# Kernel optimization log

Hardware: AMD Instinct MI355X
Metric: run time of the kernel (lower is better)

## Reference

```python
import jax, jax.numpy as jnp
import numpy as np

IN_F = 256
OUT_F = 128
ALPHA = 0.2  # LeakyReLU negative slope
NEG_INF = -9.0e15


def setup_inputs() -> dict:
    key = jax.random.key(0)
    k_h, k_j, k_adj, k_w1, k_w2, k_a = jax.random.split(key, 6)
    B, N = 8, 2048
    h = jax.random.normal(k_h, (B, N, IN_F), dtype=jnp.float32)
    j = jax.random.normal(k_j, (B, N, IN_F), dtype=jnp.float32)
    adj = jax.random.randint(k_adj, (B, N, N), 0, 2, dtype=jnp.int32)
    # xavier_uniform with gain=1.414: bound = gain * sqrt(6/(fan_in+fan_out))
    def xavier(k, shape, gain=1.414):
        bound = gain * np.sqrt(6.0 / (shape[0] + shape[1]))
        return jax.random.uniform(k, shape, jnp.float32, -bound, bound)
    W1 = xavier(k_w1, (IN_F, OUT_F))
    W2 = xavier(k_w2, (IN_F, OUT_F))
    a = xavier(k_a, (2 * OUT_F, 1))
    return {"h": h, "j": j, "adj": adj, "W1": W1, "W2": W2, "a": a}


def reference(h, j, adj, W1, W2, a):
    # Projections: [B, N, OUT_F]
    Wh = jnp.einsum("bnf,fo->bno", h, W1)
    Wj = jnp.einsum("bnf,fo->bno", j, W2)
    # Additive attention logits: e[b,i,k] = leakyrelu(Wh@a1 [i] + Wh@a2 [k])
    Wh1 = Wh @ a[:OUT_F, :]   # [B, N, 1]
    Wh2 = Wh @ a[OUT_F:, :]   # [B, N, 1]
    e = jax.nn.leaky_relu(Wh1 + jnp.swapaxes(Wh2, 1, 2), negative_slope=ALPHA)
    # Mask non-edges, row-softmax over neighbors (dim=2)
    logits = jnp.where(adj > 0, e, NEG_INF)
    attention = jax.nn.softmax(logits, axis=2)
    # dropout skipped (eval mode). attention@Wh + attention@Wj == attention@(Wh+Wj)
    output = jnp.einsum("bik,bko->bio", attention, Wh + Wj)
    return jax.nn.elu(output)  # concat=True
```

## Files before the change

### kernel.cpp

```cpp
#include <hip/hip_runtime.h>
#include <hip/hip_bf16.h>

#define BATCH 8
#define NN 2048
#define IN_F 256
#define OUT_F 128
#define ALPHA 0.2f

typedef __attribute__((ext_vector_type(8))) short short8v;
typedef __attribute__((ext_vector_type(4))) float f32x4;

static __device__ __forceinline__ unsigned short f2bf(float x) {
    unsigned int u = __float_as_uint(x);
    u = (u + 0x7fffu + ((u >> 16) & 1u)) >> 16;
    return (unsigned short)u;
}

static __device__ __forceinline__ unsigned long long pk4(float a, float b, float c, float d) {
    union { unsigned long long ll; __hip_bfloat162 h2[2]; } u;
    u.h2[0] = __float22bfloat162_rn(make_float2(a, b));
    u.h2[1] = __float22bfloat162_rn(make_float2(c, d));
    return u.ll;
}

__global__ __launch_bounds__(256) void k_prew(
    const float* __restrict__ W1, const float* __restrict__ W2,
    const float* __restrict__ a,
    unsigned short* __restrict__ Wt, float* __restrict__ w1a1, float* __restrict__ w1a2)
{
    const int t = threadIdx.x;
    const int k8 = blockIdx.x * 8;
#pragma unroll
    for (int q = 0; q < 4; ++q) {
        const int idx = q * 256 + t;
        const int o = idx & 127;
        const int kk = k8 + (idx >> 7);
        const float v = (kk < IN_F) ? W1[kk * OUT_F + o] : W2[(kk - IN_F) * OUT_F + o];
        Wt[(size_t)o * 512 + kk] = f2bf(v);
    }
    if (k8 < IN_F) {
        const int lane = t & 63, w = t >> 6;
#pragma unroll
        for (int u = 0; u < 2; ++u) {
            const int kk = k8 + 2 * w + u;
            const float* wr = W1 + kk * OUT_F;
            float v1 = wr[lane] * a[lane] + wr[lane + 64] * a[lane + 64];
            float v2 = wr[lane] * a[OUT_F + lane] + wr[lane + 64] * a[OUT_F + lane + 64];
#pragma unroll
            for (int off = 32; off; off >>= 1) {
                v1 += __shfl_xor(v1, off);
                v2 += __shfl_xor(v2, off);
            }
            if (lane == 0) { w1a1[kk] = v1; w1a2[kk] = v2; }
        }
    }
}

#define BM 16

__global__ __launch_bounds__(256) void k_proj(
    const float* __restrict__ h, const float* __restrict__ j,
    const unsigned short* __restrict__ Wt,
    const float* __restrict__ w1a1g, const float* __restrict__ w1a2g,
    const int* __restrict__ adj,
    unsigned short* __restrict__ Vf, float* __restrict__ s1, float* __restrict__ s2,
    unsigned short* __restrict__ bits16)
{
    __shared__ __align__(16) unsigned short X[BM * 512];

    const int t = threadIdx.x, lane = t & 63, w = t >> 6;
    const int row0 = blockIdx.x * BM;
    const int b = row0 >> 11, n0 = row0 & 2047;

    const float4* wa1v = (const float4*)w1a1g;
    const float4* wa2v = (const float4*)w1a2g;

    const int srow = w * 4 + (lane >> 4);
    const int scol = lane & 15;
    const int sswz = (srow & 7) << 4;
    const float* hrow = h + (size_t)(row0 + srow) * IN_F;
    const float* jrow = j + (size_t)(row0 + srow) * IN_F;

    float d1 = 0.f, d2 = 0.f;
#pragma unroll
    for (int q = 0; q < 4; ++q) {
        const int f4 = q * 16 + scol;
        const float4 hv = ((const float4*)hrow)[f4];
        *(unsigned long long*)((char*)X + ((srow * 1024 + f4 * 8) ^ sswz)) =
            pk4(hv.x, hv.y, hv.z, hv.w);
        const float4 a1 = wa1v[f4], a2 = wa2v[f4];
        d1 += hv.x * a1.x + hv.y * a1.y + hv.z * a1.z + hv.w * a1.w;
        d2 += hv.x * a2.x + hv.y * a2.y + hv.z * a2.z + hv.w * a2.w;
    }
#pragma unroll
    for (int q = 0; q < 4; ++q) {
        const int f4 = q * 16 + scol;
        const float4 jv = ((const float4*)jrow)[f4];
        *(unsigned long long*)((char*)X + ((srow * 1024 + 512 + f4 * 8) ^ sswz)) =
            pk4(jv.x, jv.y, jv.z, jv.w);
    }
    d1 += __shfl_xor(d1, 1); d1 += __shfl_xor(d1, 2);
    d1 += __shfl_xor(d1, 4); d1 += __shfl_xor(d1, 8);
    d2 += __shfl_xor(d2, 1); d2 += __shfl_xor(d2, 2);
    d2 += __shfl_xor(d2, 4); d2 += __shfl_xor(d2, 8);
    if (scol == 0) { s1[row0 + srow] = d1; s2[row0 + srow] = d2; }
    __syncthreads();

    const unsigned short* wb = Wt + (size_t)(w * 32 + (lane & 15)) * 512 + ((lane >> 4) * 8);
    const int abase = (lane & 15) * 1024 + ((lane >> 4) * 16);
    const int aswz = (lane & 7) << 4;

    f32x4 acc0 = {0.f, 0.f, 0.f, 0.f}, acc1 = {0.f, 0.f, 0.f, 0.f};
#pragma unroll
    for (int ks = 0; ks < 16; ++ks) {
        const short8v af = *(const short8v*)((const char*)X + ((abase + ks * 64) ^ aswz));
        const short8v b0 = *(const short8v*)(wb + ks * 32);
        const short8v b1 = *(const short8v*)(wb + 16 * 512 + ks * 32);
        acc0 = __builtin_amdgcn_mfma_f32_16x16x32_bf16(af, b0, acc0, 0, 0, 0);
        acc1 = __builtin_amdgcn_mfma_f32_16x16x32_bf16(af, b1, acc1, 0, 0, 0);
    }

    const int nn = n0 + (lane >> 4) * 4;
    const size_t vbase = (size_t)b * 524288
                       + ((size_t)(nn >> 5) << 13)
                       + (((nn & 31) >> 3) << 4) + ((nn & 7) << 1);
#pragma unroll
    for (int f = 0; f < 2; ++f) {
        const f32x4 ac = f ? acc1 : acc0;
        const int o = w * 32 + f * 16 + (lane & 15);
        *(unsigned long long*)((char*)Vf + vbase + o * 64) = pk4(ac[0], ac[1], ac[2], ac[3]);
    }

    const int gstride = 1024 * 256;
    for (int g = blockIdx.x * 256 + t; g < (BATCH * NN * NN) / 16; g += gstride) {
        const int4* ap = (const int4*)(adj + (size_t)g * 16);
        const int4 x0 = ap[0], x1 = ap[1], x2 = ap[2], x3 = ap[3];
        unsigned m = 0;
        m |= (x0.x > 0) ? 1u : 0u;        m |= (x0.y > 0) ? 2u : 0u;
        m |= (x0.z > 0) ? 4u : 0u;        m |= (x0.w > 0) ? 8u : 0u;
        m |= (x1.x > 0) ? 16u : 0u;       m |= (x1.y > 0) ? 32u : 0u;
        m |= (x1.z > 0) ? 64u : 0u;       m |= (x1.w > 0) ? 128u : 0u;
        m |= (x2.x > 0) ? 256u : 0u;      m |= (x2.y > 0) ? 512u : 0u;
        m |= (x2.z > 0) ? 1024u : 0u;     m |= (x2.w > 0) ? 2048u : 0u;
        m |= (x3.x > 0) ? 4096u : 0u;     m |= (x3.y > 0) ? 8192u : 0u;
        m |= (x3.z > 0) ? 16384u : 0u;    m |= (x3.w > 0) ? 32768u : 0u;
        bits16[g] = (unsigned short)m;
    }
}

#define IBLK 32

__global__ __launch_bounds__(256, 3) void k_attn(
    const unsigned char* __restrict__ bits, const unsigned short* __restrict__ Vf,
    const float* __restrict__ s1g, const float* __restrict__ s2g,
    float* __restrict__ out)
{
    __shared__ __align__(16) char smem[33792];
    __shared__ float rs_lds[4][IBLK];
    __shared__ float wmaxs[4];
    __shared__ __align__(16) float lut[16][4];

    float* s2_lds = (float*)smem;
    unsigned int* bitw = (unsigned int*)(smem + 8192);
    float* comb = (float*)smem;

    const int t = threadIdx.x, lane = t & 63, w = t >> 6;
    const int orig = blockIdx.x;
    const int b = orig & 7;
    const int r = orig >> 3;
    const int oh = r >> 6;
    const int i0 = (r & 63) * IBLK;

    if (t < 16) {
        lut[t][0] = (float)(t & 1);
        lut[t][1] = (float)((t >> 1) & 1);
        lut[t][2] = (float)((t >> 2) & 1);
        lut[t][3] = (float)((t >> 3) & 1);
    }

    {
        const unsigned int* bg = (const unsigned int*)(bits + ((size_t)b * NN + i0) * 256);
#pragma unroll
        for (int q = 0; q < 8; ++q) {
            const int idx = q * 256 + t;
            bitw[(idx >> 6) * 65 + (idx & 63)] = bg[idx];
        }
    }

    const float4* s2v = (const float4*)(s2g + b * NN);
    float lmax = -1e30f;
#pragma unroll
    for (int q = 0; q < 2; ++q) {
        const int idx = q * 256 + t;
        const float4 v = s2v[idx];
        ((float4*)s2_lds)[idx] = v;
        lmax = fmaxf(fmaxf(lmax, fmaxf(v.x, v.y)), fmaxf(v.z, v.w));
    }
#pragma unroll
    for (int off = 32; off; off >>= 1) lmax = fmaxf(lmax, __shfl_xor(lmax, off));
    if (lane == 0) wmaxs[w] = lmax;

    const int irow = lane & 15;
    const int kcb = lane >> 4;
    const int kw = w * 512;

    const float s1r0 = s1g[b * NN + i0 + irow];
    const float s1r1 = s1g[b * NN + i0 + 16 + irow];
    __syncthreads();
    const float s2max = fmaxf(fmaxf(wmaxs[0], wmaxs[1]), fmaxf(wmaxs[2], wmaxs[3]));
    const float mx0 = s1r0 + s2max, mx1 = s1r1 + s2max;
    const float mA0 = fmaxf(mx0, ALPHA * mx0);
    const float mA1 = fmaxf(mx1, ALPHA * mx1);

    const float* s2p = s2_lds + kw + kcb * 8;
    const char* vfb = (const char*)Vf + (size_t)b * 524288 + (size_t)(w * 16) * 8192
                    + (size_t)(oh * 64 + irow) * 64 + (size_t)kcb * 16;
    const unsigned int* bw0p = bitw + irow * 65 + w * 16;
    const unsigned int* bw1p = bitw + (16 + irow) * 65 + w * 16;

    short8v vone;
#pragma unroll
    for (int q = 0; q < 8; ++q) vone[q] = (short)0x3F80;

    f32x4 acc0[4], acc1[4];
    f32x4 acc_ps0 = {0.f, 0.f, 0.f, 0.f}, acc_ps1 = {0.f, 0.f, 0.f, 0.f};
#pragma unroll
    for (int og = 0; og < 4; ++og) {
        acc0[og] = (f32x4){0.f, 0.f, 0.f, 0.f};
        acc1[og] = (f32x4){0.f, 0.f, 0.f, 0.f};
    }

#pragma unroll
    for (int ks = 0; ks < 16; ++ks) {
        const char* vk = vfb + (size_t)ks * 8192;
        const short8v vf0 = *(const short8v*)(vk);
        const short8v vf1 = *(const short8v*)(vk + 1024);
        const short8v vf2 = *(const short8v*)(vk + 2048);
        const short8v vf3 = *(const short8v*)(vk + 3072);

        const unsigned int bb0 = (bw0p[ks] >> (kcb * 8)) & 0xffu;
        const unsigned int bb1 = (bw1p[ks] >> (kcb * 8)) & 0xffu;
        const float4 m00 = ((const float4*)lut)[bb0 & 15], m01 = ((const float4*)lut)[bb0 >> 4];
        const float4 m10 = ((const float4*)lut)[bb1 & 15], m11 = ((const float4*)lut)[bb1 >> 4];

        const float4 sa = *(const float4*)(s2p + ks * 32);
        const float4 sb = *(const float4*)(s2p + ks * 32 + 4);
        const float s2r[8] = {sa.x, sa.y, sa.z, sa.w, sb.x, sb.y, sb.z, sb.w};
        const float mk0[8] = {m00.x, m00.y, m00.z, m00.w, m01.x, m01.y, m01.z, m01.w};
        const float mk1[8] = {m10.x, m10.y, m10.z, m10.w, m11.x, m11.y, m11.z, m11.w};

        float p0[8], p1[8];
#pragma unroll
        for (int e = 0; e < 8; ++e) {
            float x0 = s1r0 + s2r[e];
            x0 = fmaxf(x0, ALPHA * x0);
            p0[e] = __expf(x0 - mA0) * mk0[e];
            float x1 = s1r1 + s2r[e];
            x1 = fmaxf(x1, ALPHA * x1);
            p1[e] = __expf(x1 - mA1) * mk1[e];
        }
        union { short8v v; __hip_bfloat162 h2[4]; } pb0, pb1;
#pragma unroll
        for (int q = 0; q < 4; ++q) {
            pb0.h2[q] = __float22bfloat162_rn(make_float2(p0[2 * q], p0[2 * q + 1]));
            pb1.h2[q] = __float22bfloat162_rn(make_float2(p1[2 * q], p1[2 * q + 1]));
        }

        acc_ps0 = __builtin_amdgcn_mfma_f32_16x16x32_bf16(vone, pb0.v, acc_ps0, 0, 0, 0);
        acc_ps1 = __builtin_amdgcn_mfma_f32_16x16x32_bf16(vone, pb1.v, acc_ps1, 0, 0, 0);
        acc0[0] = __builtin_amdgcn_mfma_f32_16x16x32_bf16(vf0, pb0.v, acc0[0], 0, 0, 0);
        acc1[0] = __builtin_amdgcn_mfma_f32_16x16x32_bf16(vf0, pb1.v, acc1[0], 0, 0, 0);
        acc0[1] = __builtin_amdgcn_mfma_f32_16x16x32_bf16(vf1, pb0.v, acc0[1], 0, 0, 0);
        acc1[1] = __builtin_amdgcn_mfma_f32_16x16x32_bf16(vf1, pb1.v, acc1[1], 0, 0, 0);
        acc0[2] = __builtin_amdgcn_mfma_f32_16x16x32_bf16(vf2, pb0.v, acc0[2], 0, 0, 0);
        acc1[2] = __builtin_amdgcn_mfma_f32_16x16x32_bf16(vf2, pb1.v, acc1[2], 0, 0, 0);
        acc0[3] = __builtin_amdgcn_mfma_f32_16x16x32_bf16(vf3, pb0.v, acc0[3], 0, 0, 0);
        acc1[3] = __builtin_amdgcn_mfma_f32_16x16x32_bf16(vf3, pb1.v, acc1[3], 0, 0, 0);
    }

    if (lane < 16) {
        rs_lds[w][lane] = acc_ps0[0];
        rs_lds[w][16 + lane] = acc_ps1[0];
    }

    __syncthreads();
#pragma unroll
    for (int og = 0; og < 4; ++og) {
#pragma unroll
        for (int rr = 0; rr < 4; ++rr) {
            const int ol = og * 16 + kcb * 4 + rr;
            comb[(w * 64 + ol) * 33 + irow] = acc0[og][rr];
            comb[(w * 64 + ol) * 33 + 16 + irow] = acc1[og][rr];
        }
    }
    __syncthreads();

    const int i = t >> 3, oc = t & 7;
    const float tot = rs_lds[0][i] + rs_lds[1][i] + rs_lds[2][i] + rs_lds[3][i];
    const float inv = 1.0f / tot;
    float res[8];
#pragma unroll
    for (int u = 0; u < 8; ++u) {
        const int ol = oc * 8 + u;
        float v = comb[ol * 33 + i] + comb[(64 + ol) * 33 + i]
                + comb[(128 + ol) * 33 + i] + comb[(192 + ol) * 33 + i];
        v *= inv;
        res[u] = (v > 0.f) ? v : expm1f(v);
    }
    float4* ob = (float4*)(out + ((size_t)b * NN + i0 + i) * OUT_F + oh * 64 + oc * 8);
    ob[0] = make_float4(res[0], res[1], res[2], res[3]);
    ob[1] = make_float4(res[4], res[5], res[6], res[7]);
}

extern "C" void kernel_launch(void* const* d_in, const int* in_sizes, int n_in,
                              void* d_out, int out_size, void* d_ws, size_t ws_size,
                              hipStream_t stream) {
    const float* h  = (const float*)d_in[0];
    const float* j  = (const float*)d_in[1];
    const int* adj  = (const int*)d_in[2];
    const float* W1 = (const float*)d_in[3];
    const float* W2 = (const float*)d_in[4];
    const float* a  = (const float*)d_in[5];
    float* out = (float*)d_out;

    char* ws = (char*)d_ws;
    unsigned short* Vf = (unsigned short*)ws;
    ws += (size_t)BATCH * OUT_F * NN * 2;
    float* s1 = (float*)ws; ws += (size_t)BATCH * NN * 4;
    float* s2 = (float*)ws; ws += (size_t)BATCH * NN * 4;
    unsigned short* Wt = (unsigned short*)ws; ws += 128 * 512 * 2;
    float* w1a1 = (float*)ws; ws += 512 * 4;
    float* w1a2 = (float*)ws; ws += 512 * 4;
    unsigned char* bits = (unsigned char*)ws;

    k_prew<<<64, 256, 0, stream>>>(W1, W2, a, Wt, w1a1, w1a2);
    k_proj<<<(BATCH * NN) / BM, 256, 0, stream>>>(h, j, Wt, w1a1, w1a2, adj,
                                                  Vf, s1, s2, (unsigned short*)bits);
    k_attn<<<(BATCH * NN) / IBLK * 2, 256, 0, stream>>>(bits, Vf, s1, s2, out);
}
```

Baseline: 68.74 us.

## Double attention row tile to 64 rows per block, reusing V fragments

Each attention block now covers 64 query rows instead of 32, so every V fragment loaded from global memory feeds four row groups of MFMAs instead of two. The aim is to halve V traffic per output and amortise the shared s2 and bitmask setup over more rows. The cost is twice the accumulator registers, occupancy hint lowered from 3 to 2 blocks, and an epilogue that reduces through LDS in two serialized passes with extra barriers. This relies on the launch grid shrinking to match the new row indexing.

After: 70.80 us. +3.0%, slower.

```diff
diff --git a/kernel.cpp b/kernel.cpp
--- a/kernel.cpp
+++ b/kernel.cpp
@@ -148,9 +148,9 @@
     }
 }
 
-#define IBLK 32
-
-__global__ __launch_bounds__(256, 3) void k_attn(
+#define IBLK 64
+
+__global__ __launch_bounds__(256, 2) void k_attn(
     const unsigned char* __restrict__ bits, const unsigned short* __restrict__ Vf,
     const float* __restrict__ s1g, const float* __restrict__ s2g,
     float* __restrict__ out)
@@ -168,8 +168,8 @@
     const int orig = blockIdx.x;
     const int b = orig & 7;
     const int r = orig >> 3;
-    const int oh = r >> 6;
-    const int i0 = (r & 63) * IBLK;
+    const int oh = r >> 5;
+    const int i0 = (r & 31) * IBLK;
 
     if (t < 16) {
         lut[t][0] = (float)(t & 1);
@@ -181,7 +181,7 @@
     {
         const unsigned int* bg = (const unsigned int*)(bits + ((size_t)b * NN + i0) * 256);
 #pragma unroll
-        for (int q = 0; q < 8; ++q) {
+        for (int q = 0; q < 16; ++q) {
             const int idx = q * 256 + t;
             bitw[(idx >> 6) * 65 + (idx & 63)] = bg[idx];
         }
@@ -204,30 +204,39 @@
     const int kcb = lane >> 4;
     const int kw = w * 512;
 
-    const float s1r0 = s1g[b * NN + i0 + irow];
-    const float s1r1 = s1g[b * NN + i0 + 16 + irow];
+    const float* s1b = s1g + b * NN + i0 + irow;
+    const float s1r0 = s1b[0], s1r1 = s1b[16], s1r2 = s1b[32], s1r3 = s1b[48];
     __syncthreads();
     const float s2max = fmaxf(fmaxf(wmaxs[0], wmaxs[1]), fmaxf(wmaxs[2], wmaxs[3]));
     const float mx0 = s1r0 + s2max, mx1 = s1r1 + s2max;
+    const float mx2 = s1r2 + s2max, mx3 = s1r3 + s2max;
     const float mA0 = fmaxf(mx0, ALPHA * mx0);
     const float mA1 = fmaxf(mx1, ALPHA * mx1);
+    const float mA2 = fmaxf(mx2, ALPHA * mx2);
+    const float mA3 = fmaxf(mx3, ALPHA * mx3);
 
     const float* s2p = s2_lds + kw + kcb * 8;
     const char* vfb = (const char*)Vf + (size_t)b * 524288 + (size_t)(w * 16) * 8192
                     + (size_t)(oh * 64 + irow) * 64 + (size_t)kcb * 16;
-    const unsigned int* bw0p = bitw + irow * 65 + w * 16;
-    const unsigned int* bw1p = bitw + (16 + irow) * 65 + w * 16;
+    const unsigned int* bwp0 = bitw + (irow) * 65 + w * 16;
+    const unsigned int* bwp1 = bitw + (16 + irow) * 65 + w * 16;
+    const unsigned int* bwp2 = bitw + (32 + irow) * 65 + w * 16;
+    const unsigned int* bwp3 = bitw + (48 + irow) * 65 + w * 16;
+    const int sh = kcb * 8;
 
     short8v vone;
 #pragma unroll
     for (int q = 0; q < 8; ++q) vone[q] = (short)0x3F80;
 
-    f32x4 acc0[4], acc1[4];
-    f32x4 acc_ps0 = {0.f, 0.f, 0.f, 0.f}, acc_ps1 = {0.f, 0.f, 0.f, 0.f};
+    f32x4 acc0[4], acc1[4], acc2[4], acc3[4];
+    f32x4 ps0 = {0.f, 0.f, 0.f, 0.f}, ps1 = {0.f, 0.f, 0.f, 0.f};
+    f32x4 ps2 = {0.f, 0.f, 0.f, 0.f}, ps3 = {0.f, 0.f, 0.f, 0.f};
 #pragma unroll
     for (int og = 0; og < 4; ++og) {
         acc0[og] = (f32x4){0.f, 0.f, 0.f, 0.f};
         acc1[og] = (f32x4){0.f, 0.f, 0.f, 0.f};
+        acc2[og] = (f32x4){0.f, 0.f, 0.f, 0.f};
+        acc3[og] = (f32x4){0.f, 0.f, 0.f, 0.f};
     }
 
 #pragma unroll
@@ -238,52 +247,111 @@
         const short8v vf2 = *(const short8v*)(vk + 2048);
         const short8v vf3 = *(const short8v*)(vk + 3072);
 
-        const unsigned int bb0 = (bw0p[ks] >> (kcb * 8)) & 0xffu;
-        const unsigned int bb1 = (bw1p[ks] >> (kcb * 8)) & 0xffu;
-        const float4 m00 = ((const float4*)lut)[bb0 & 15], m01 = ((const float4*)lut)[bb0 >> 4];
-        const float4 m10 = ((const float4*)lut)[bb1 & 15], m11 = ((const float4*)lut)[bb1 >> 4];
+        const unsigned bb0 = (bwp0[ks] >> sh) & 0xffu;
+        const unsigned bb1 = (bwp1[ks] >> sh) & 0xffu;
+        const unsigned bb2 = (bwp2[ks] >> sh) & 0xffu;
+        const unsigned bb3 = (bwp3[ks] >> sh) & 0xffu;
 
         const float4 sa = *(const float4*)(s2p + ks * 32);
         const float4 sb = *(const float4*)(s2p + ks * 32 + 4);
         const float s2r[8] = {sa.x, sa.y, sa.z, sa.w, sb.x, sb.y, sb.z, sb.w};
-        const float mk0[8] = {m00.x, m00.y, m00.z, m00.w, m01.x, m01.y, m01.z, m01.w};
-        const float mk1[8] = {m10.x, m10.y, m10.z, m10.w, m11.x, m11.y, m11.z, m11.w};
-
-        float p0[8], p1[8];
+
+        float lr[8];
 #pragma unroll
         for (int e = 0; e < 8; ++e) {
-            float x0 = s1r0 + s2r[e];
-            x0 = fmaxf(x0, ALPHA * x0);
-            p0[e] = __expf(x0 - mA0) * mk0[e];
-            float x1 = s1r1 + s2r[e];
-            x1 = fmaxf(x1, ALPHA * x1);
-            p1[e] = __expf(x1 - mA1) * mk1[e];
-        }
-        union { short8v v; __hip_bfloat162 h2[4]; } pb0, pb1;
-#pragma unroll
-        for (int q = 0; q < 4; ++q) {
-            pb0.h2[q] = __float22bfloat162_rn(make_float2(p0[2 * q], p0[2 * q + 1]));
-            pb1.h2[q] = __float22bfloat162_rn(make_float2(p1[2 * q], p1[2 * q + 1]));
-        }
-
-        acc_ps0 = __builtin_amdgcn_mfma_f32_16x16x32_bf16(vone, pb0.v, acc_ps0, 0, 0, 0);
-        acc_ps1 = __builtin_amdgcn_mfma_f32_16x16x32_bf16(vone, pb1.v, acc_ps1, 0, 0, 0);
+            const float x = s2r[e];
+            lr[e] = x;
+        }
+
+        union { short8v v; __hip_bfloat162 h2[4]; } pb0, pb1, pb2, pb3;
+        {
+            const float4 m0 = ((const float4*)lut)[bb0 & 15], m1 = ((const float4*)lut)[bb0 >> 4];
+            const float mk[8] = {m0.x, m0.y, m0.z, m0.w, m1.x, m1.y, m1.z, m1.w};
+            float p[8];
+#pragma unroll
+            for (int e = 0; e < 8; ++e) {
+                float x = s1r0 + lr[e];
+                x = fmaxf(x, ALPHA * x);
+                p[e] = __expf(x - mA0) * mk[e];
+            }
+#pragma unroll
+            for (int q = 0; q < 4; ++q)
+                pb0.h2[q] = __float22bfloat162_rn(make_float2(p[2 * q], p[2 * q + 1]));
+        }
+        {
+            const float4 m0 = ((const float4*)lut)[bb1 & 15], m1 = ((const float4*)lut)[bb1 >> 4];
+            const float mk[8] = {m0.x, m0.y, m0.z, m0.w, m1.x, m1.y, m1.z, m1.w};
+            float p[8];
+#pragma unroll
+            for (int e = 0; e < 8; ++e) {
+                float x = s1r1 + lr[e];
+                x = fmaxf(x, ALPHA * x);
+                p[e] = __expf(x - mA1) * mk[e];
+            }
+#pragma unroll
+            for (int q = 0; q < 4; ++q)
+                pb1.h2[q] = __float22bfloat162_rn(make_float2(p[2 * q], p[2 * q + 1]));
+        }
+        {
+            const float4 m0 = ((const float4*)lut)[bb2 & 15], m1 = ((const float4*)lut)[bb2 >> 4];
+            const float mk[8] = {m0.x, m0.y, m0.z, m0.w, m1.x, m1.y, m1.z, m1.w};
+            float p[8];
+#pragma unroll
+            for (int e = 0; e < 8; ++e) {
+                float x = s1r2 + lr[e];
+                x = fmaxf(x, ALPHA * x);
+                p[e] = __expf(x - mA2) * mk[e];
+            }
+#pragma unroll
+            for (int q = 0; q < 4; ++q)
+                pb2.h2[q] = __float22bfloat162_rn(make_float2(p[2 * q], p[2 * q + 1]));
+        }
+        {
+            const float4 m0 = ((const float4*)lut)[bb3 & 15], m1 = ((const float4*)lut)[bb3 >> 4];
+            const float mk[8] = {m0.x, m0.y, m0.z, m0.w, m1.x, m1.y, m1.z, m1.w};
+            float p[8];
+#pragma unroll
+            for (int e = 0; e < 8; ++e) {
+                float x = s1r3 + lr[e];
+                x = fmaxf(x, ALPHA * x);
+                p[e] = __expf(x - mA3) * mk[e];
+            }
+#pragma unroll
+            for (int q = 0; q < 4; ++q)
+                pb3.h2[q] = __float22bfloat162_rn(make_float2(p[2 * q], p[2 * q + 1]));
+        }
+
+        ps0 = __builtin_amdgcn_mfma_f32_16x16x32_bf16(vone, pb0.v, ps0, 0, 0, 0);
+        ps1 = __builtin_amdgcn_mfma_f32_16x16x32_bf16(vone, pb1.v, ps1, 0, 0, 0);
+        ps2 = __builtin_amdgcn_mfma_f32_16x16x32_bf16(vone, pb2.v, ps2, 0, 0, 0);
+        ps3 = __builtin_amdgcn_mfma_f32_16x16x32_bf16(vone, pb3.v, ps3, 0, 0, 0);
         acc0[0] = __builtin_amdgcn_mfma_f32_16x16x32_bf16(vf0, pb0.v, acc0[0], 0, 0, 0);
         acc1[0] = __builtin_amdgcn_mfma_f32_16x16x32_bf16(vf0, pb1.v, acc1[0], 0, 0, 0);
+        acc2[0] = __builtin_amdgcn_mfma_f32_16x16x32_bf16(vf0, pb2.v, acc2[0], 0, 0, 0);
+        acc3[0] = __builtin_amdgcn_mfma_f32_16x16x32_bf16(vf0, pb3.v, acc3[0], 0, 0, 0);
         acc0[1] = __builtin_amdgcn_mfma_f32_16x16x32_bf16(vf1, pb0.v, acc0[1], 0, 0, 0);
         acc1[1] = __builtin_amdgcn_mfma_f32_16x16x32_bf16(vf1, pb1.v, acc1[1], 0, 0, 0);
+        acc2[1] = __builtin_amdgcn_mfma_f32_16x16x32_bf16(vf1, pb2.v, acc2[1], 0, 0, 0);
+        acc3[1] = __builtin_amdgcn_mfma_f32_16x16x32_bf16(vf1, pb3.v, acc3[1], 0, 0, 0);
         acc0[2] = __builtin_amdgcn_mfma_f32_16x16x32_bf16(vf2, pb0.v, acc0[2], 0, 0, 0);
         acc1[2] = __builtin_amdgcn_mfma_f32_16x16x32_bf16(vf2, pb1.v, acc1[2], 0, 0, 0);
+        acc2[2] = __builtin_amdgcn_mfma_f32_16x16x32_bf16(vf2, pb2.v, acc2[2], 0, 0, 0);
+        acc3[2] = __builtin_amdgcn_mfma_f32_16x16x32_bf16(vf2, pb3.v, acc3[2], 0, 0, 0);
         acc0[3] = __builtin_amdgcn_mfma_f32_16x16x32_bf16(vf3, pb0.v, acc0[3], 0, 0, 0);
         acc1[3] = __builtin_amdgcn_mfma_f32_16x16x32_bf16(vf3, pb1.v, acc1[3], 0, 0, 0);
+        acc2[3] = __builtin_amdgcn_mfma_f32_16x16x32_bf16(vf3, pb2.v, acc2[3], 0, 0, 0);
+        acc3[3] = __builtin_amdgcn_mfma_f32_16x16x32_bf16(vf3, pb3.v, acc3[3], 0, 0, 0);
     }
 
     if (lane < 16) {
-        rs_lds[w][lane] = acc_ps0[0];
-        rs_lds[w][16 + lane] = acc_ps1[0];
-    }
-
-    __syncthreads();
+        rs_lds[w][irow]      = ps0[0];
+        rs_lds[w][16 + irow] = ps1[0];
+        rs_lds[w][32 + irow] = ps2[0];
+        rs_lds[w][48 + irow] = ps3[0];
+    }
+
+    __syncthreads();
+
 #pragma unroll
     for (int og = 0; og < 4; ++og) {
 #pragma unroll
@@ -294,22 +362,53 @@
         }
     }
     __syncthreads();
-
-    const int i = t >> 3, oc = t & 7;
-    const float tot = rs_lds[0][i] + rs_lds[1][i] + rs_lds[2][i] + rs_lds[3][i];
-    const float inv = 1.0f / tot;
-    float res[8];
-#pragma unroll
-    for (int u = 0; u < 8; ++u) {
-        const int ol = oc * 8 + u;
-        float v = comb[ol * 33 + i] + comb[(64 + ol) * 33 + i]
-                + comb[(128 + ol) * 33 + i] + comb[(192 + ol) * 33 + i];
-        v *= inv;
-        res[u] = (v > 0.f) ? v : expm1f(v);
-    }
-    float4* ob = (float4*)(out + ((size_t)b * NN + i0 + i) * OUT_F + oh * 64 + oc * 8);
-    ob[0] = make_float4(res[0], res[1], res[2], res[3]);
-    ob[1] = make_float4(res[4], res[5], res[6], res[7]);
+    {
+        const int i = t >> 3, oc = t & 7;
+        const float tot = rs_lds[0][i] + rs_lds[1][i] + rs_lds[2][i] + rs_lds[3][i];
+        const float inv = 1.0f / tot;
+        float res[8];
+#pragma unroll
+        for (int u = 0; u < 8; ++u) {
+            const int ol = oc * 8 + u;
+            float v = comb[ol * 33 + i] + comb[(64 + ol) * 33 + i]
+                    + comb[(128 + ol) * 33 + i] + comb[(192 + ol) * 33 + i];
+            v *= inv;
+            res[u] = (v > 0.f) ? v : expm1f(v);
+        }
+        float4* ob = (float4*)(out + ((size_t)b * NN + i0 + i) * OUT_F + oh * 64 + oc * 8);
+        ob[0] = make_float4(res[0], res[1], res[2], res[3]);
+        ob[1] = make_float4(res[4], res[5], res[6], res[7]);
+    }
+    __syncthreads();
+
+#pragma unroll
+    for (int og = 0; og < 4; ++og) {
+#pragma unroll
+        for (int rr = 0; rr < 4; ++rr) {
+            const int ol = og * 16 + kcb * 4 + rr;
+            comb[(w * 64 + ol) * 33 + irow] = acc2[og][rr];
+            comb[(w * 64 + ol) * 33 + 16 + irow] = acc3[og][rr];
+        }
+    }
+    __syncthreads();
+    {
+        const int i = t >> 3, oc = t & 7;
+        const float tot = rs_lds[0][32 + i] + rs_lds[1][32 + i]
+                        + rs_lds[2][32 + i] + rs_lds[3][32 + i];
+        const float inv = 1.0f / tot;
+        float res[8];
+#pragma unroll
+        for (int u = 0; u < 8; ++u) {
+            const int ol = oc * 8 + u;
+            float v = comb[ol * 33 + i] + comb[(64 + ol) * 33 + i]
+                    + comb[(128 + ol) * 33 + i] + comb[(192 + ol) * 33 + i];
+            v *= inv;
+            res[u] = (v > 0.f) ? v : expm1f(v);
+        }
+        float4* ob = (float4*)(out + ((size_t)b * NN + i0 + 32 + i) * OUT_F + oh * 64 + oc * 8);
+        ob[0] = make_float4(res[0], res[1], res[2], res[3]);
+        ob[1] = make_float4(res[4], res[5], res[6], res[7]);
+    }
 }
 
 extern "C" void kernel_launch(void* const* d_in, const int* in_sizes, int n_in,
```
